# Kernel tuning notes

Measured on AMD Instinct MI355X. Metric: run time of the kernel, lower is better.

The kernel has to match this reference:

```python
import jax, jax.numpy as jnp
import numpy as np
import math

B, S, D, H, M = 2, 2048, 1024, 16, 64
HD = D // H  # head_dim = 64


def setup_inputs() -> dict:
    key = jax.random.key(0)
    ks = jax.random.split(key, 16)
    inp = {
        "query": jax.random.normal(ks[0], (B, S, D), jnp.float32),
        "key": jax.random.normal(ks[1], (B, S, D), jnp.float32),
        "value": jax.random.normal(ks[2], (B, S, D), jnp.float32),
        "mask": jax.random.randint(ks[3], (B, 1, 1, S), 0, 2, jnp.int32),
        "Wq": jax.random.normal(ks[4], (D, D), jnp.float32) * 0.02,
        "bq": jnp.zeros((D,), jnp.float32),
        "Wk": jax.random.normal(ks[5], (D, D), jnp.float32) * 0.02,
        "bk": jnp.zeros((D,), jnp.float32),
        "Wv": jax.random.normal(ks[6], (D, D), jnp.float32) * 0.02,
        "bv": jnp.zeros((D,), jnp.float32),
        "Wo": jax.random.normal(ks[7], (D, D), jnp.float32) * 0.02,
        "bo": jnp.zeros((D,), jnp.float32),
        "m_k": jax.random.normal(ks[8], (1, M, D), jnp.float32) * (1.0 / HD),
        "m_v": jax.random.normal(ks[9], (1, M, D), jnp.float32) * (1.0 / M),
    }
    return inp


def reference(query, key, value, mask, Wq, bq, Wk, bk, Wv, bv, Wo, bo, m_k, m_v):
    b, nq, d = query.shape
    nk = key.shape[1]
    h, hd, m = H, HD, M
    scale = math.sqrt(hd)

    Q = query @ Wq.T + bq                      # [b, nq, d]
    K = key @ Wk.T + bk                        # [b, nk, d]
    V = value @ Wv.T + bv                      # [b, nk, d]

    mk = scale * jnp.broadcast_to(m_k, (b, m, d))           # sqrt(head_dim)*m_k
    mv = math.sqrt(m) * jnp.broadcast_to(m_v, (b, m, d))    # sqrt(m)*m_v

    K = jnp.concatenate([K, mk], axis=1)       # [b, nk+m, d]
    V = jnp.concatenate([V, mv], axis=1)

    Qh = Q.reshape(b, nq, h, hd).transpose(0, 2, 1, 3)           # [b,h,nq,hd]
    Kh = K.reshape(b, nk + m, h, hd).transpose(0, 2, 1, 3)       # [b,h,nk+m,hd]
    Vh = V.reshape(b, nk + m, h, hd).transpose(0, 2, 1, 3)

    energy = jnp.einsum('bhqd,bhkd->bhqk', Qh, Kh) / scale       # [b,h,nq,nk+m]
    # mask only the first nk key columns; memory slots are never masked
    masked = jnp.where(mask == 0, jnp.float32(-1e20), energy[..., :nk])
    energy = jnp.concatenate([masked, energy[..., nk:]], axis=-1)

    attention = jax.nn.softmax(energy, axis=-1)
    x = jnp.einsum('bhqk,bhkd->bhqd', attention, Vh)             # [b,h,nq,hd]
    x = x.transpose(0, 2, 1, 3).reshape(b, nq, d)
    return x @ Wo.T + bo
```

## Files before the change

kernel.cpp:

```cpp
#include <hip/hip_runtime.h>
#include <hip/hip_bf16.h>
#include <stdint.h>

#define B_  2
#define S_  2048
#define D_  1024
#define H_  16
#define HD_ 64
#define M_  64
#define SKM (S_ + M_)
#define LOG2E 1.44269504088896340736f

typedef __attribute__((ext_vector_type(8))) short s16x8;
typedef __attribute__((ext_vector_type(4))) float f32x4;
typedef __attribute__((ext_vector_type(16))) float f32x16;

#define GLOAD16(gp, lp) __builtin_amdgcn_global_load_lds( \
    (const __attribute__((address_space(1))) void*)(gp),  \
    (__attribute__((address_space(3))) void*)(lp), 16, 0, 0)

#define WAITVM(N) do { asm volatile("s_waitcnt vmcnt(" #N ")" ::: "memory"); \
                       __builtin_amdgcn_sched_barrier(0); } while (0)
#define BARRIER() do { asm volatile("" ::: "memory"); \
                       __builtin_amdgcn_s_barrier(); \
                       asm volatile("" ::: "memory"); } while (0)

__device__ __forceinline__ unsigned short f2bf(float f) {
  union { float f; unsigned int u; } v; v.f = f;
  unsigned int r = v.u + 0x7fffu + ((v.u >> 16) & 1u);
  return (unsigned short)(r >> 16);
}

__device__ __forceinline__ unsigned pkbf(float lo, float hi) {
  union { __hip_bfloat162 b; unsigned u; } t;
  t.b = __float22bfloat162_rn(make_float2(lo, hi));
  return t.u;
}

__global__ void compact_mask(const int* __restrict__ mask,
                             int* __restrict__ idx, int* __restrict__ cnt) {
  const int b = blockIdx.x;
  __shared__ int base, wsum[4];
  if (threadIdx.x == 0) base = 0;
  const int lane = threadIdx.x & 63, w = threadIdx.x >> 6;
  __syncthreads();
  for (int c = 0; c < S_; c += 256) {
    int key = c + threadIdx.x;
    int mv = mask[b * S_ + key];
    unsigned long long bal = __ballot(mv != 0);
    int pre = __popcll(bal & ((1ull << lane) - 1ull));
    if (lane == 0) wsum[w] = __popcll(bal);
    __syncthreads();
    int woff = 0;
    for (int i = 0; i < w; i++) woff += wsum[i];
    int tot = wsum[0] + wsum[1] + wsum[2] + wsum[3];
    if (mv) idx[b * S_ + base + woff + pre] = key;
    __syncthreads();
    if (threadIdx.x == 0) base += tot;
    __syncthreads();
  }
  if (threadIdx.x == 0) cnt[b] = base;
}

__global__ void cvt_all(const float* __restrict__ q,
                        const float* __restrict__ w0, const float* __restrict__ w1,
                        const float* __restrict__ w2, const float* __restrict__ w3,
                        unsigned short* __restrict__ qf,
                        unsigned short* __restrict__ o0, unsigned short* __restrict__ o1,
                        unsigned short* __restrict__ o2, unsigned short* __restrict__ o3) {
  size_t i = ((size_t)blockIdx.x * 256 + threadIdx.x) * 4;
  const float* in; unsigned short* out; size_t off;
  const size_t NQs = (size_t)B_ * S_ * D_;
  if (i < NQs) { in = q; out = qf; off = i; }
  else {
    size_t j = i - NQs;
    int wsel = (int)(j >> 20);
    off = j & ((1u << 20) - 1);
    in  = (wsel == 0) ? w0 : (wsel == 1) ? w1 : (wsel == 2) ? w2 : w3;
    out = (wsel == 0) ? o0 : (wsel == 1) ? o1 : (wsel == 2) ? o2 : o3;
  }
  float4 v = *(const float4*)&in[off];
  ushort4 o;
  o.x = f2bf(v.x); o.y = f2bf(v.y); o.z = f2bf(v.z); o.w = f2bf(v.w);
  *(ushort4*)&out[off] = o;
}

__global__ void cvt_kv_gather(const float* __restrict__ key, const float* __restrict__ value,
                              unsigned short* __restrict__ kf, unsigned short* __restrict__ vf,
                              const int* __restrict__ idx, const int* __restrict__ cnt) {
  int b = blockIdx.y, j = blockIdx.x;
  if (j >= cnt[b]) return;
  const float* in = blockIdx.z ? value : key;
  unsigned short* out = blockIdx.z ? vf : kf;
  int src = idx[b * S_ + j];
  const float* ip = in + ((size_t)(b * S_) + src) * D_;
  unsigned short* op = out + ((size_t)(b * S_) + j) * D_;
  int t = threadIdx.x * 4;
  float4 v = *(const float4*)&ip[t];
  ushort4 o;
  o.x = f2bf(v.x); o.y = f2bf(v.y); o.z = f2bf(v.z); o.w = f2bf(v.w);
  *(ushort4*)&op[t] = o;
}

__global__ void fill_mem(const float* __restrict__ mk, const float* __restrict__ mv,
                         unsigned short* __restrict__ Kb, unsigned short* __restrict__ VtG,
                         const int* __restrict__ cnt) {
  int i = blockIdx.x * 256 + threadIdx.x;
  int row = i >> 10, col = i & 1023;
  int hI = col >> 6, dd = col & 63;
  unsigned short kv = f2bf(8.0f * mk[i]);
  unsigned short vv = f2bf(8.0f * mv[i]);
#pragma unroll
  for (int b = 0; b < B_; b++) {
    int c = cnt[b];
    Kb[((size_t)(b * SKM) + c + row) * D_ + col] = kv;
    VtG[((size_t)(b * H_ + hI) * HD_ + dd) * SKM + c + row] = vv;
  }
}

__device__ __forceinline__ void gemm_core4(
    const unsigned short* __restrict__ A,
    const unsigned short* __restrict__ Bw,
    unsigned short* As, unsigned short* Bs,
    int mBase, int nBase, int K,
    int w, int lane, int wr, int wc, int lr, int lk,
    f32x4 acc[4][4]) {
  const int srow = w * 32 + (lane >> 2);
  const int cd = lane & 3;
  const int NT = K / 32;

#define STAGE_(buf, k0)                                                          \
  {                                                                              \
    _Pragma("unroll")                                                            \
    for (int i = 0; i < 2; i++) {                                                \
      int r = srow + i * 16;                                                     \
      int ca = cd ^ ((r >> 1) & 3);           \
      GLOAD16(&A[(size_t)(mBase + r) * K + (k0) + ca * 8],                       \
              &As[(buf) * (128 * 32) + (w * 32 + i * 16) * 32]);                 \
      GLOAD16(&Bw[(size_t)(nBase + r) * K + (k0) + ca * 8],                      \
              &Bs[(buf) * (128 * 32) + (w * 32 + i * 16) * 32]);                 \
    }                                                                            \
  }

  STAGE_(0, 0);
  STAGE_(1, 32);
  STAGE_(2, 64);
  for (int t = 0; t < NT; ++t) {
    const int cur = t & 3;
    if (t + 3 < NT) {
      STAGE_((t + 3) & 3, (t + 3) * 32);
      WAITVM(12);
    } else if (t + 3 == NT) {
      WAITVM(8);
    } else if (t + 2 == NT) {
      WAITVM(4);
    } else {
      WAITVM(0);
    }
    BARRIER();
    s16x8 af[4], bf[4];
#pragma unroll
    for (int mi = 0; mi < 4; mi++) {
      int row = wr * 64 + mi * 16 + lr;
      af[mi] = *(const s16x8*)&As[cur * (128 * 32) + row * 32 + ((lk ^ ((row >> 1) & 3)) << 3)];
    }
#pragma unroll
    for (int ni = 0; ni < 4; ni++) {
      int row = wc * 64 + ni * 16 + lr;
      bf[ni] = *(const s16x8*)&Bs[cur * (128 * 32) + row * 32 + ((lk ^ ((row >> 1) & 3)) << 3)];
    }
#pragma unroll
    for (int mi = 0; mi < 4; mi++)
#pragma unroll
      for (int ni = 0; ni < 4; ni++)
        acc[mi][ni] = __builtin_amdgcn_mfma_f32_16x16x32_bf16(af[mi], bf[ni], acc[mi][ni], 0, 0, 0);
    BARRIER();
  }
#undef STAGE_
}

__global__ __launch_bounds__(256)
void gemm_qkv(const unsigned short* __restrict__ qf, const unsigned short* __restrict__ kf,
              const unsigned short* __restrict__ vf,
              const unsigned short* __restrict__ wq, const unsigned short* __restrict__ wk,
              const unsigned short* __restrict__ wv,
              const float* __restrict__ bq, const float* __restrict__ bk,
              const float* __restrict__ bv,
              unsigned short* __restrict__ Qb, unsigned short* __restrict__ Kb,
              unsigned short* __restrict__ Vt,
              const int* __restrict__ cnt) {
  __shared__ __align__(16) unsigned short As[4 * 128 * 32];
  __shared__ __align__(16) unsigned short Bs[4 * 128 * 32];
  const int z = blockIdx.x >> 8;
  const int local = blockIdx.x & 255;
  const int ws = (local & 7) * 32 + (local >> 3);
  const int nBase = (ws & 7) * 128, mBase = (ws >> 3) * 128;
  if (z) {
    int c = (mBase < S_) ? cnt[0] : cnt[1];
    int lo = (mBase < S_) ? mBase : (mBase - S_);
    if (lo >= c) return;
  }
  const unsigned short* A  = (z == 0) ? qf : (z == 1) ? kf : vf;
  const unsigned short* Bw = (z == 0) ? wq : (z == 1) ? wk : wv;
  const float* bias        = (z == 0) ? bq : (z == 1) ? bk : bv;

  const int tid = threadIdx.x, lane = tid & 63;
  const int w = tid >> 6, wr = w >> 1, wc = w & 1;
  const int lr = lane & 15, lk = lane >> 4;

  const f32x4 fz = {0.f, 0.f, 0.f, 0.f};
  f32x4 acc[4][4];
#pragma unroll
  for (int i = 0; i < 4; i++)
#pragma unroll
    for (int j = 0; j < 4; j++) acc[i][j] = fz;

  gemm_core4(A, Bw, As, Bs, mBase, nBase, D_, w, lane, wr, wc, lr, lk, acc);

  const float alpha = (z == 0) ? 0.125f * LOG2E : 1.0f;
#pragma unroll
  for (int mi = 0; mi < 4; mi++)
#pragma unroll
    for (int ni = 0; ni < 4; ni++)
#pragma unroll
      for (int r = 0; r < 4; r++) {
        int gr = mBase + wr * 64 + mi * 16 + lk * 4 + r;
        int gc = nBase + wc * 64 + ni * 16 + lr;
        float v = (acc[mi][ni][r] + bias[gc]) * alpha;
        if (z == 2) {
          int bb = gr / S_, s = gr - bb * S_;
          int hI = gc >> 6, dd = gc & 63;
          Vt[((size_t)(bb * H_ + hI) * HD_ + dd) * SKM + s] = f2bf(v);
        } else if (z == 1) {
          int orow = gr + (gr / S_) * M_;
          Kb[(size_t)orow * D_ + gc] = f2bf(v);
        } else {
          Qb[(size_t)gr * D_ + gc] = f2bf(v);
        }
      }
}

__global__ __launch_bounds__(256)
void gemm_o(const unsigned short* __restrict__ A, const unsigned short* __restrict__ Bw,
            const float* __restrict__ bias, float* __restrict__ Cout) {
  __shared__ __align__(16) unsigned short As[4 * 128 * 32];
  __shared__ __align__(16) unsigned short Bs[4 * 128 * 32];
  const int local = blockIdx.x & 255;
  const int ws = (local & 7) * 32 + (local >> 3);
  const int nBase = (ws & 7) * 128, mBase = (ws >> 3) * 128;
  const int tid = threadIdx.x, lane = tid & 63;
  const int w = tid >> 6, wr = w >> 1, wc = w & 1;
  const int lr = lane & 15, lk = lane >> 4;

  const f32x4 fz = {0.f, 0.f, 0.f, 0.f};
  f32x4 acc[4][4];
#pragma unroll
  for (int i = 0; i < 4; i++)
#pragma unroll
    for (int j = 0; j < 4; j++) acc[i][j] = fz;

  gemm_core4(A, Bw, As, Bs, mBase, nBase, D_, w, lane, wr, wc, lr, lk, acc);

#pragma unroll
  for (int mi = 0; mi < 4; mi++)
#pragma unroll
    for (int ni = 0; ni < 4; ni++)
#pragma unroll
      for (int r = 0; r < 4; r++) {
        int gr = mBase + wr * 64 + mi * 16 + lk * 4 + r;
        int gc = nBase + wc * 64 + ni * 16 + lr;
        Cout[(size_t)gr * D_ + gc] = acc[mi][ni][r] + bias[gc];
      }
}

__global__ __launch_bounds__(512)
void attn_kernel(const unsigned short* __restrict__ Qb,
                 const unsigned short* __restrict__ Kb,
                 const unsigned short* __restrict__ VtG,
                 const int* __restrict__ cnt,
                 unsigned short* __restrict__ Xb) {
  __shared__ __align__(16) unsigned short Ks[64 * 64];
  __shared__ __align__(16) unsigned short Vs[64 * 64];

  const int tid = threadIdx.x, lane = tid & 63, w = tid >> 6;
  const int l31 = lane & 31, hh = lane >> 5;
  const int qt = blockIdx.x, h = blockIdx.y, b = blockIdx.z;

  const int total = cnt[b] + M_;
  const int nt = (total + 63) >> 6;

  const int r0 = tid >> 3, c0 = tid & 7;
  const int ck = c0 ^ (r0 & 7);
  const unsigned short* Kg = Kb + (size_t)b * SKM * D_ + (size_t)h * HD_;
  const unsigned short* Vg = VtG + (size_t)(b * H_ + h) * HD_ * SKM;

  const unsigned short* qp = Qb + ((size_t)(b * S_) + qt * 256 + w * 32 + l31) * D_ + h * HD_;
  s16x8 qf[4];
#pragma unroll
  for (int ds = 0; ds < 4; ds++) qf[ds] = *(const s16x8*)&qp[ds * 16 + hh * 8];

  f32x16 accO[2];
#pragma unroll
  for (int dt = 0; dt < 2; dt++)
#pragma unroll
    for (int j = 0; j < 16; j++) accO[dt][j] = 0.f;
  float m_r = -1e20f, l_r = 0.f;

  uint4 kr0, vr0;
  auto LOAD = [&](int kt) {
    kr0 = *(const uint4*)&Kg[(size_t)(kt * 64 + r0) * D_ + c0 * 8];
    vr0 = *(const uint4*)&Vg[(size_t)r0 * SKM + kt * 64 + c0 * 8];
  };
  LOAD(0);

  for (int kt = 0; kt < nt; ++kt) {
    __syncthreads();
    *(uint4*)&Ks[r0 * 64 + ck * 8] = kr0;
    *(uint4*)&Vs[r0 * 64 + ck * 8] = vr0;
    __syncthreads();
    if (kt + 1 < nt) LOAD(kt + 1);

    f32x16 p0, p1;
#pragma unroll
    for (int j = 0; j < 16; j++) { p0[j] = 0.f; p1[j] = 0.f; }
#pragma unroll
    for (int ds = 0; ds < 4; ds++) {
      s16x8 ka0 = *(const s16x8*)&Ks[l31 * 64 + (((ds * 2 + hh) ^ (l31 & 7)) << 3)];
      s16x8 ka1 = *(const s16x8*)&Ks[(32 + l31) * 64 + (((ds * 2 + hh) ^ (l31 & 7)) << 3)];
      p0 = __builtin_amdgcn_mfma_f32_32x32x16_bf16(ka0, qf[ds], p0, 0, 0, 0);
      p1 = __builtin_amdgcn_mfma_f32_32x32x16_bf16(ka1, qf[ds], p1, 0, 0, 0);
    }

    if (kt == nt - 1) {
      int valid = total - kt * 64;
#pragma unroll
      for (int j = 0; j < 16; j++) {
        int kl = (j & 3) + 8 * (j >> 2) + 4 * hh;
        if (kl >= valid) p0[j] = -1e30f;
        if (kl + 32 >= valid) p1[j] = -1e30f;
      }
    }

    float vmax = fmaxf(p0[0], p1[0]);
#pragma unroll
    for (int j = 1; j < 16; j++) vmax = fmaxf(vmax, fmaxf(p0[j], p1[j]));
    vmax = fmaxf(vmax, __shfl_xor(vmax, 32));
    if (!__all(vmax - m_r <= 8.0f)) {
      float mnew = fmaxf(m_r, vmax);
      float fac = __builtin_amdgcn_exp2f(m_r - mnew);
      m_r = mnew;
      l_r *= fac;
#pragma unroll
      for (int dt = 0; dt < 2; dt++)
#pragma unroll
        for (int j = 0; j < 16; j++) accO[dt][j] *= fac;
    }
    float sum = 0.f;
#pragma unroll
    for (int j = 0; j < 16; j++) {
      p0[j] = __builtin_amdgcn_exp2f(p0[j] - m_r); sum += p0[j];
      p1[j] = __builtin_amdgcn_exp2f(p1[j] - m_r); sum += p1[j];
    }
    sum += __shfl_xor(sum, 32);
    l_r += sum;

    s16x8 pf_[4];
#pragma unroll
    for (int ks = 0; ks < 4; ks++) {
      const int base = (ks & 1) * 8;
#define ELT(t) ((ks >= 2) ? p1[base + (t)] : p0[base + (t)])
      unsigned w0 = pkbf(ELT(0), ELT(1));
      unsigned w1 = pkbf(ELT(2), ELT(3));
      unsigned w2 = pkbf(ELT(4), ELT(5));
      unsigned w3 = pkbf(ELT(6), ELT(7));
#undef ELT
      unsigned s0 = hh ? w0 : w2;
      unsigned s1 = hh ? w1 : w3;
      unsigned g0 = (unsigned)__shfl_xor((int)s0, 32);
      unsigned g1 = (unsigned)__shfl_xor((int)s1, 32);
      union { s16x8 v; unsigned u[4]; } pf;
      pf.u[0] = hh ? g0 : w0;
      pf.u[1] = hh ? g1 : w1;
      pf.u[2] = hh ? w2 : g0;
      pf.u[3] = hh ? w3 : g1;
      pf_[ks] = pf.v;
    }

#pragma unroll
    for (int dt = 0; dt < 2; dt++)
#pragma unroll
      for (int ks = 0; ks < 4; ks++) {
        s16x8 va = *(const s16x8*)&Vs[(dt * 32 + l31) * 64 + (((ks * 2 + hh) ^ (l31 & 7)) << 3)];
        accO[dt] = __builtin_amdgcn_mfma_f32_32x32x16_bf16(va, pf_[ks], accO[dt], 0, 0, 0);
      }
  }

  float invl = 1.0f / l_r;
  size_t orow = ((size_t)(b * S_) + qt * 256 + w * 32 + l31) * D_ + h * HD_;
#pragma unroll
  for (int dt = 0; dt < 2; dt++)
#pragma unroll
    for (int j = 0; j < 16; j++) {
      int d = dt * 32 + (j & 3) + 8 * (j >> 2) + 4 * hh;
      Xb[orow + d] = f2bf(accO[dt][j] * invl);
    }
}

extern "C" void kernel_launch(void* const* d_in, const int* in_sizes, int n_in,
                              void* d_out, int out_size, void* d_ws, size_t ws_size,
                              hipStream_t stream) {
  const float* query = (const float*)d_in[0];
  const float* key   = (const float*)d_in[1];
  const float* value = (const float*)d_in[2];
  const int*   mask  = (const int*)d_in[3];
  const float* Wq    = (const float*)d_in[4];
  const float* bq    = (const float*)d_in[5];
  const float* Wk    = (const float*)d_in[6];
  const float* bk    = (const float*)d_in[7];
  const float* Wv    = (const float*)d_in[8];
  const float* bv    = (const float*)d_in[9];
  const float* Wo    = (const float*)d_in[10];
  const float* bo    = (const float*)d_in[11];
  const float* m_k   = (const float*)d_in[12];
  const float* m_v   = (const float*)d_in[13];

  const int NQ = B_ * S_ * D_;
  const int NW = D_ * D_;
  const int NK = B_ * SKM * D_;

  unsigned short* ws = (unsigned short*)d_ws;
  unsigned short* qf = ws;
  unsigned short* kf = qf + NQ;
  unsigned short* vf = kf + NQ;
  unsigned short* wq = vf + NQ;
  unsigned short* wk = wq + NW;
  unsigned short* wv = wk + NW;
  unsigned short* wo = wv + NW;
  unsigned short* Qb = wo + NW;
  unsigned short* Kb = Qb + NQ;
  unsigned short* Vt = Kb + NK;
  unsigned short* Xb = Vt + NK;
  int* idx = (int*)(Xb + NQ);
  int* cnt = idx + B_ * S_;

  compact_mask<<<B_, 256, 0, stream>>>(mask, idx, cnt);
  cvt_kv_gather<<<dim3(S_, B_, 2), 256, 0, stream>>>(key, value, kf, vf, idx, cnt);
  cvt_all<<<(NQ + 4 * NW) / 1024, 256, 0, stream>>>(query, Wq, Wk, Wv, Wo,
                                                    qf, wq, wk, wv, wo);

  gemm_qkv<<<768, 256, 0, stream>>>(qf, kf, vf, wq, wk, wv, bq, bk, bv, Qb, Kb, Vt, cnt);
  fill_mem<<<(M_ * D_) / 256, 256, 0, stream>>>(m_k, m_v, Kb, Vt, cnt);

  attn_kernel<<<dim3(S_ / 256, H_, B_), 512, 0, stream>>>(Qb, Kb, Vt, cnt, Xb);

  gemm_o<<<256, 256, 0, stream>>>(Xb, wo, bo, (float*)d_out);
}
```

Measured before the change: 141.3 us.

## Fuse conversion kernels, switch GEMMs to double buffering, add MFMA priority hints

Merges the activation/weight conversion and the masked K/V gather-convert into one launch, removing a kernel launch boundary. Replaces the 4-stage LDS pipeline in the GEMM core with a 2-stage double buffer that waits for all loads each iteration, halving shared memory per block, which may raise occupancy but exposes more load latency. Adds s_setprio around MFMA blocks in the GEMMs and the attention kernel to favour matrix issue. Also simplifies batch index arithmetic in the QKV epilogue.

```diff
diff --git a/kernel.cpp b/kernel.cpp
--- a/kernel.cpp
+++ b/kernel.cpp
@@ -62,44 +62,47 @@
   if (threadIdx.x == 0) cnt[b] = base;
 }
 
-__global__ void cvt_all(const float* __restrict__ q,
-                        const float* __restrict__ w0, const float* __restrict__ w1,
-                        const float* __restrict__ w2, const float* __restrict__ w3,
-                        unsigned short* __restrict__ qf,
-                        unsigned short* __restrict__ o0, unsigned short* __restrict__ o1,
-                        unsigned short* __restrict__ o2, unsigned short* __restrict__ o3) {
-  size_t i = ((size_t)blockIdx.x * 256 + threadIdx.x) * 4;
-  const float* in; unsigned short* out; size_t off;
+__global__ void cvt_fused(const float* __restrict__ q,
+                          const float* __restrict__ w0, const float* __restrict__ w1,
+                          const float* __restrict__ w2, const float* __restrict__ w3,
+                          const float* __restrict__ key, const float* __restrict__ value,
+                          unsigned short* __restrict__ qf,
+                          unsigned short* __restrict__ o0, unsigned short* __restrict__ o1,
+                          unsigned short* __restrict__ o2, unsigned short* __restrict__ o3,
+                          unsigned short* __restrict__ kf, unsigned short* __restrict__ vf,
+                          const int* __restrict__ idx, const int* __restrict__ cnt) {
   const size_t NQs = (size_t)B_ * S_ * D_;
-  if (i < NQs) { in = q; out = qf; off = i; }
-  else {
-    size_t j = i - NQs;
-    int wsel = (int)(j >> 20);
-    off = j & ((1u << 20) - 1);
-    in  = (wsel == 0) ? w0 : (wsel == 1) ? w1 : (wsel == 2) ? w2 : w3;
-    out = (wsel == 0) ? o0 : (wsel == 1) ? o1 : (wsel == 2) ? o2 : o3;
-  }
-  float4 v = *(const float4*)&in[off];
-  ushort4 o;
-  o.x = f2bf(v.x); o.y = f2bf(v.y); o.z = f2bf(v.z); o.w = f2bf(v.w);
-  *(ushort4*)&out[off] = o;
-}
-
-__global__ void cvt_kv_gather(const float* __restrict__ key, const float* __restrict__ value,
-                              unsigned short* __restrict__ kf, unsigned short* __restrict__ vf,
-                              const int* __restrict__ idx, const int* __restrict__ cnt) {
-  int b = blockIdx.y, j = blockIdx.x;
-  if (j >= cnt[b]) return;
-  const float* in = blockIdx.z ? value : key;
-  unsigned short* out = blockIdx.z ? vf : kf;
-  int src = idx[b * S_ + j];
-  const float* ip = in + ((size_t)(b * S_) + src) * D_;
-  unsigned short* op = out + ((size_t)(b * S_) + j) * D_;
-  int t = threadIdx.x * 4;
-  float4 v = *(const float4*)&ip[t];
-  ushort4 o;
-  o.x = f2bf(v.x); o.y = f2bf(v.y); o.z = f2bf(v.z); o.w = f2bf(v.w);
-  *(ushort4*)&op[t] = o;
+  if (blockIdx.x < 8192) {
+    size_t i = ((size_t)blockIdx.x * 256 + threadIdx.x) * 4;
+    const float* in; unsigned short* out; size_t off;
+    if (i < NQs) { in = q; out = qf; off = i; }
+    else {
+      size_t j = i - NQs;
+      int wsel = (int)(j >> 20);
+      off = j & ((1u << 20) - 1);
+      in  = (wsel == 0) ? w0 : (wsel == 1) ? w1 : (wsel == 2) ? w2 : w3;
+      out = (wsel == 0) ? o0 : (wsel == 1) ? o1 : (wsel == 2) ? o2 : o3;
+    }
+    float4 v = *(const float4*)&in[off];
+    ushort4 o;
+    o.x = f2bf(v.x); o.y = f2bf(v.y); o.z = f2bf(v.z); o.w = f2bf(v.w);
+    *(ushort4*)&out[off] = o;
+  } else {
+    int gid = blockIdx.x - 8192;
+    int kv = gid >> 12, rem = gid & 4095;
+    int b = rem >> 11, j = rem & 2047;
+    if (j >= cnt[b]) return;
+    const float* in = kv ? value : key;
+    unsigned short* out = kv ? vf : kf;
+    int src = idx[b * S_ + j];
+    const float* ip = in + ((size_t)(b * S_) + src) * D_;
+    unsigned short* op = out + ((size_t)(b * S_) + j) * D_;
+    int t = threadIdx.x * 4;
+    float4 v = *(const float4*)&ip[t];
+    ushort4 o;
+    o.x = f2bf(v.x); o.y = f2bf(v.y); o.z = f2bf(v.z); o.w = f2bf(v.w);
+    *(ushort4*)&op[t] = o;
+  }
 }
 
 __global__ void fill_mem(const float* __restrict__ mk, const float* __restrict__ mv,
@@ -118,7 +121,7 @@
   }
 }
 
-__device__ __forceinline__ void gemm_core4(
+__device__ __forceinline__ void gemm_core2(
     const unsigned short* __restrict__ A,
     const unsigned short* __restrict__ Bw,
     unsigned short* As, unsigned short* Bs,
@@ -143,21 +146,11 @@
   }
 
   STAGE_(0, 0);
-  STAGE_(1, 32);
-  STAGE_(2, 64);
+  WAITVM(0);
+  BARRIER();
+  int cur = 0;
   for (int t = 0; t < NT; ++t) {
-    const int cur = t & 3;
-    if (t + 3 < NT) {
-      STAGE_((t + 3) & 3, (t + 3) * 32);
-      WAITVM(12);
-    } else if (t + 3 == NT) {
-      WAITVM(8);
-    } else if (t + 2 == NT) {
-      WAITVM(4);
-    } else {
-      WAITVM(0);
-    }
-    BARRIER();
+    if (t + 1 < NT) STAGE_(cur ^ 1, (t + 1) * 32);
     s16x8 af[4], bf[4];
 #pragma unroll
     for (int mi = 0; mi < 4; mi++) {
@@ -169,12 +162,16 @@
       int row = wc * 64 + ni * 16 + lr;
       bf[ni] = *(const s16x8*)&Bs[cur * (128 * 32) + row * 32 + ((lk ^ ((row >> 1) & 3)) << 3)];
     }
+    __builtin_amdgcn_s_setprio(1);
 #pragma unroll
     for (int mi = 0; mi < 4; mi++)
 #pragma unroll
       for (int ni = 0; ni < 4; ni++)
         acc[mi][ni] = __builtin_amdgcn_mfma_f32_16x16x32_bf16(af[mi], bf[ni], acc[mi][ni], 0, 0, 0);
+    __builtin_amdgcn_s_setprio(0);
+    WAITVM(0);
     BARRIER();
+    cur ^= 1;
   }
 #undef STAGE_
 }
@@ -189,16 +186,15 @@
               unsigned short* __restrict__ Qb, unsigned short* __restrict__ Kb,
               unsigned short* __restrict__ Vt,
               const int* __restrict__ cnt) {
-  __shared__ __align__(16) unsigned short As[4 * 128 * 32];
-  __shared__ __align__(16) unsigned short Bs[4 * 128 * 32];
+  __shared__ __align__(16) unsigned short As[2 * 128 * 32];
+  __shared__ __align__(16) unsigned short Bs[2 * 128 * 32];
   const int z = blockIdx.x >> 8;
   const int local = blockIdx.x & 255;
-  const int ws = (local & 7) * 32 + (local >> 3);
-  const int nBase = (ws & 7) * 128, mBase = (ws >> 3) * 128;
+  const int wsz = (local & 7) * 32 + (local >> 3);
+  const int nBase = (wsz & 7) * 128, mBase = (wsz >> 3) * 128;
+  const int bb = (mBase >= S_);
   if (z) {
-    int c = (mBase < S_) ? cnt[0] : cnt[1];
-    int lo = (mBase < S_) ? mBase : (mBase - S_);
-    if (lo >= c) return;
+    if (mBase - bb * S_ >= cnt[bb]) return;
   }
   const unsigned short* A  = (z == 0) ? qf : (z == 1) ? kf : vf;
   const unsigned short* Bw = (z == 0) ? wq : (z == 1) ? wk : wv;
@@ -215,7 +211,7 @@
 #pragma unroll
     for (int j = 0; j < 4; j++) acc[i][j] = fz;
 
-  gemm_core4(A, Bw, As, Bs, mBase, nBase, D_, w, lane, wr, wc, lr, lk, acc);
+  gemm_core2(A, Bw, As, Bs, mBase, nBase, D_, w, lane, wr, wc, lr, lk, acc);
 
   const float alpha = (z == 0) ? 0.125f * LOG2E : 1.0f;
 #pragma unroll
@@ -228,11 +224,11 @@
         int gc = nBase + wc * 64 + ni * 16 + lr;
         float v = (acc[mi][ni][r] + bias[gc]) * alpha;
         if (z == 2) {
-          int bb = gr / S_, s = gr - bb * S_;
+          int s = gr - bb * S_;
           int hI = gc >> 6, dd = gc & 63;
           Vt[((size_t)(bb * H_ + hI) * HD_ + dd) * SKM + s] = f2bf(v);
         } else if (z == 1) {
-          int orow = gr + (gr / S_) * M_;
+          int orow = gr + bb * M_;
           Kb[(size_t)orow * D_ + gc] = f2bf(v);
         } else {
           Qb[(size_t)gr * D_ + gc] = f2bf(v);
@@ -243,11 +239,11 @@
 __global__ __launch_bounds__(256)
 void gemm_o(const unsigned short* __restrict__ A, const unsigned short* __restrict__ Bw,
             const float* __restrict__ bias, float* __restrict__ Cout) {
-  __shared__ __align__(16) unsigned short As[4 * 128 * 32];
-  __shared__ __align__(16) unsigned short Bs[4 * 128 * 32];
+  __shared__ __align__(16) unsigned short As[2 * 128 * 32];
+  __shared__ __align__(16) unsigned short Bs[2 * 128 * 32];
   const int local = blockIdx.x & 255;
-  const int ws = (local & 7) * 32 + (local >> 3);
-  const int nBase = (ws & 7) * 128, mBase = (ws >> 3) * 128;
+  const int wsz = (local & 7) * 32 + (local >> 3);
+  const int nBase = (wsz & 7) * 128, mBase = (wsz >> 3) * 128;
   const int tid = threadIdx.x, lane = tid & 63;
   const int w = tid >> 6, wr = w >> 1, wc = w & 1;
   const int lr = lane & 15, lk = lane >> 4;
@@ -259,7 +255,7 @@
 #pragma unroll
     for (int j = 0; j < 4; j++) acc[i][j] = fz;
 
-  gemm_core4(A, Bw, As, Bs, mBase, nBase, D_, w, lane, wr, wc, lr, lk, acc);
+  gemm_core2(A, Bw, As, Bs, mBase, nBase, D_, w, lane, wr, wc, lr, lk, acc);
 
 #pragma unroll
   for (int mi = 0; mi < 4; mi++)
@@ -323,6 +319,7 @@
     f32x16 p0, p1;
 #pragma unroll
     for (int j = 0; j < 16; j++) { p0[j] = 0.f; p1[j] = 0.f; }
+    __builtin_amdgcn_s_setprio(1);
 #pragma unroll
     for (int ds = 0; ds < 4; ds++) {
       s16x8 ka0 = *(const s16x8*)&Ks[l31 * 64 + (((ds * 2 + hh) ^ (l31 & 7)) << 3)];
@@ -330,6 +327,7 @@
       p0 = __builtin_amdgcn_mfma_f32_32x32x16_bf16(ka0, qf[ds], p0, 0, 0, 0);
       p1 = __builtin_amdgcn_mfma_f32_32x32x16_bf16(ka1, qf[ds], p1, 0, 0, 0);
     }
+    __builtin_amdgcn_s_setprio(0);
 
     if (kt == nt - 1) {
       int valid = total - kt * 64;
@@ -386,6 +384,7 @@
       pf_[ks] = pf.v;
     }
 
+    __builtin_amdgcn_s_setprio(1);
 #pragma unroll
     for (int dt = 0; dt < 2; dt++)
 #pragma unroll
@@ -393,6 +392,7 @@
         s16x8 va = *(const s16x8*)&Vs[(dt * 32 + l31) * 64 + (((ks * 2 + hh) ^ (l31 & 7)) << 3)];
         accO[dt] = __builtin_amdgcn_mfma_f32_32x32x16_bf16(va, pf_[ks], accO[dt], 0, 0, 0);
       }
+    __builtin_amdgcn_s_setprio(0);
   }
 
   float invl = 1.0f / l_r;
@@ -444,9 +444,8 @@
   int* cnt = idx + B_ * S_;
 
   compact_mask<<<B_, 256, 0, stream>>>(mask, idx, cnt);
-  cvt_kv_gather<<<dim3(S_, B_, 2), 256, 0, stream>>>(key, value, kf, vf, idx, cnt);
-  cvt_all<<<(NQ + 4 * NW) / 1024, 256, 0, stream>>>(query, Wq, Wk, Wv, Wo,
-                                                    qf, wq, wk, wv, wo);
+  cvt_fused<<<16384, 256, 0, stream>>>(query, Wq, Wk, Wv, Wo, key, value,
+                                       qf, wq, wk, wv, wo, kf, vf, idx, cnt);
 
   gemm_qkv<<<768, 256, 0, stream>>>(qf, kf, vf, wq, wk, wv, bq, bk, bv, Qb, Kb, Vt, cnt);
   fill_mem<<<(M_ * D_) / 256, 256, 0, stream>>>(m_k, m_v, Kb, Vt, cnt);
```

After: 134.7 us. 4.7% less time.
